# Performance work log

Hardware: AMD Instinct MI355X
Metric: run time of the kernel (lower is better)

Reference implementation:

```python
import jax, jax.numpy as jnp
import numpy as np

BN_EPS = 1e-5

def mish(x):
    return x * jnp.tanh(jax.nn.softplus(x))

def gconv1x1(x, w, b):
    # x: [b, c, h, w]; w: [g, cg, cg] block-diagonal 1x1 grouped conv; b: [c]
    bs, c, h, wd = x.shape
    g, cg, _ = w.shape
    xr = x.reshape(bs, g, cg, h * wd)
    y = jnp.einsum('goi,bgin->bgon', w, xr).reshape(bs, c, h, wd)
    return y + b[None, :, None, None]

def setup_inputs() -> dict:
    key = jax.random.key(0)
    ks = jax.random.split(key, 10)
    bs, c, h, w = 4, 256, 64, 64
    g = 4
    cg = c // g
    s = 0.05
    return {
        'rgb': jax.random.normal(ks[0], (bs, c, h, w), jnp.float32),
        'ir': jax.random.normal(ks[1], (bs, c, h, w), jnp.float32),
        'w_q': jax.random.normal(ks[2], (g, cg, cg), jnp.float32) * s,
        'b_q': jax.random.normal(ks[3], (c,), jnp.float32) * s,
        'w_k': jax.random.normal(ks[4], (g, cg, cg), jnp.float32) * s,
        'b_k': jax.random.normal(ks[5], (c,), jnp.float32) * s,
        'w_v': jax.random.normal(ks[6], (g, cg, cg), jnp.float32) * s,
        'b_v': jax.random.normal(ks[7], (c,), jnp.float32) * s,
        'w4': jax.random.normal(ks[8], (c, c), jnp.float32) * s,
        'b4': jax.random.normal(ks[9], (c,), jnp.float32) * s,
        'gamma': jnp.ones((c,), jnp.float32),
        'beta': jnp.zeros((c,), jnp.float32),
        'rmean': jnp.zeros((c,), jnp.float32),
        'rvar': jnp.ones((c,), jnp.float32),
    }

def reference(rgb, ir, w_q, b_q, w_k, b_k, w_v, b_v, w4, b4, gamma, beta, rmean, rvar):
    bs, c, h, w = rgb.shape
    scale = c ** (-0.5)
    q = gconv1x1(rgb, w_q, b_q).reshape(bs, c, h * w)   # [b, c, n]
    k = gconv1x1(ir, w_k, b_k).reshape(bs, c, h * w)    # [b, c, n]
    v = gconv1x1(ir, w_v, b_v).reshape(bs, c, h * w)    # [b, c, n]
    # attn[b, i, j] = sum_c q[b, c, i] * k[b, c, j]
    attn = jnp.einsum('bci,bcj->bij', q, k) * scale     # [b, n, n]
    attn = jax.nn.softmax(attn, axis=-1)
    z = jnp.einsum('bij,bcj->bci', attn, v)             # [b, c, n]
    z = z.reshape(bs, c, h, w)
    # conv4: full 1x1 conv + BatchNorm (eval stats) + Mish
    y = jnp.einsum('oc,bchw->bohw', w4, z) + b4[None, :, None, None]
    inv = gamma * jax.lax.rsqrt(rvar + BN_EPS)
    y = y * inv[None, :, None, None] + (beta - rmean * inv)[None, :, None, None]
    return rgb + mish(y)
```

## Files before the change

kernel.cpp:

```cpp
#include <hip/hip_runtime.h>
#include <stdint.h>
#include <stddef.h>

typedef short short8 __attribute__((ext_vector_type(8)));
typedef short short4v __attribute__((ext_vector_type(4)));
typedef float f32x4 __attribute__((ext_vector_type(4)));
typedef float f32x16 __attribute__((ext_vector_type(16)));
typedef unsigned int u32x4 __attribute__((ext_vector_type(4)));

#define MFMA16(a, b, c) __builtin_amdgcn_mfma_f32_16x16x32_bf16(a, b, c, 0, 0, 0)
#define MFMA32(a, b, c) __builtin_amdgcn_mfma_f32_32x32x16_bf16(a, b, c, 0, 0, 0)
#define P32SWAP(a, b) asm("v_permlane32_swap_b32 %0, %1" : "+v"(a), "+v"(b))

static constexpr int B = 4, C = 256, CG = 64, N = 4096;

__device__ __forceinline__ unsigned short f2bf(float f) {
  unsigned int u = __builtin_bit_cast(unsigned int, f);
  u += 0x7FFFu + ((u >> 16) & 1u);
  return (unsigned short)(u >> 16);
}

__device__ __forceinline__ void async16(const void* g, void* l) {
  __builtin_amdgcn_global_load_lds(
      (const __attribute__((address_space(1))) unsigned int*)g,
      (__attribute__((address_space(3))) unsigned int*)l, 16, 0, 0);
}

__global__ __launch_bounds__(256) void qkv_kernel(
    const float* __restrict__ rgb, const float* __restrict__ ir,
    const float* __restrict__ wq, const float* __restrict__ bq,
    const float* __restrict__ wk, const float* __restrict__ bk,
    const float* __restrict__ wvv, const float* __restrict__ bvv,
    unsigned short* __restrict__ qT, unsigned short* __restrict__ kT,
    unsigned short* __restrict__ vN) {
  __shared__ unsigned char xTs[256 * 144];
  __shared__ unsigned char wls[64 * 144];

  const int tid = threadIdx.x;
  const int which = blockIdx.z;
  const int bg = blockIdx.y;
  const int b = bg >> 2, g = bg & 3;
  const int n0 = blockIdx.x * 256;

  const float* x = (which == 0) ? rgb : ir;
  const float* w = (which == 0) ? wq : (which == 1 ? wk : wvv);
  const float* bias = (which == 0) ? bq : (which == 1 ? bk : bvv);

  {
    const int p = tid >> 3;
    const int nlo = (tid & 7) * 4;
    const float* r0 = x + ((size_t)(b * C + g * CG + 2 * p) * N + n0 + nlo);
    const float* r1 = r0 + N;
#pragma unroll
    for (int seg = 0; seg < 8; seg++) {
      f32x4 a = *(const f32x4*)(r0 + seg * 32);
      f32x4 c2 = *(const f32x4*)(r1 + seg * 32);
#pragma unroll
      for (int e = 0; e < 4; e++) {
        unsigned int pk =
            (unsigned int)f2bf(a[e]) | ((unsigned int)f2bf(c2[e]) << 16);
        *(unsigned int*)(xTs + (size_t)(seg * 32 + nlo + e) * 144 + 4 * p) = pk;
      }
    }
  }
  {
    const int o = tid >> 2;
    const int cs = (tid & 3) * 16;
    const float* wr = w + (size_t)g * CG * CG + (size_t)o * CG + cs;
#pragma unroll
    for (int i = 0; i < 8; i++) {
      unsigned int pk = (unsigned int)f2bf(wr[2 * i]) |
                        ((unsigned int)f2bf(wr[2 * i + 1]) << 16);
      *(unsigned int*)(wls + (size_t)o * 144 + (cs + 2 * i) * 2) = pk;
    }
  }
  __syncthreads();

  const int wv_ = tid >> 6, lane = tid & 63, l15 = lane & 15, g16 = lane >> 4;
  const f32x4 zero4 = {0.f, 0.f, 0.f, 0.f};
  f32x4 acc[4][4];
#pragma unroll
  for (int i = 0; i < 4; i++)
#pragma unroll
    for (int j = 0; j < 4; j++) acc[i][j] = zero4;

  if (which < 2) {
#pragma unroll
    for (int kk = 0; kk < 2; kk++) {
      short8 af[4], bfr[4];
#pragma unroll
      for (int mt = 0; mt < 4; mt++)
        af[mt] = *(const short8*)(xTs +
                                  (size_t)(wv_ * 64 + mt * 16 + l15) * 144 +
                                  (kk * 32 + 8 * g16) * 2);
#pragma unroll
      for (int nt = 0; nt < 4; nt++)
        bfr[nt] = *(const short8*)(wls + (size_t)(nt * 16 + l15) * 144 +
                                   (kk * 32 + 8 * g16) * 2);
#pragma unroll
      for (int mt = 0; mt < 4; mt++)
#pragma unroll
        for (int nt = 0; nt < 4; nt++)
          acc[mt][nt] = MFMA16(af[mt], bfr[nt], acc[mt][nt]);
    }
    unsigned short* out = (which == 0) ? qT : kT;
    const float qs = (which == 0) ? 0.0625f : 1.0f;
#pragma unroll
    for (int mt = 0; mt < 4; mt++)
#pragma unroll
      for (int nt = 0; nt < 4; nt++)
#pragma unroll
        for (int r = 0; r < 4; r++) {
          int nl = wv_ * 64 + mt * 16 + 4 * g16 + r;
          int co = nt * 16 + l15;
          float val = (acc[mt][nt][r] + bias[g * CG + co]) * qs;
          out[(size_t)(b * N + n0 + nl) * C + g * CG + co] = f2bf(val);
        }
  } else {
#pragma unroll
    for (int kk = 0; kk < 2; kk++) {
      short8 af[4], bfr[4];
#pragma unroll
      for (int mt = 0; mt < 4; mt++)
        af[mt] = *(const short8*)(wls + (size_t)(mt * 16 + l15) * 144 +
                                  (kk * 32 + 8 * g16) * 2);
#pragma unroll
      for (int nt = 0; nt < 4; nt++)
        bfr[nt] = *(const short8*)(xTs +
                                   (size_t)(wv_ * 64 + nt * 16 + l15) * 144 +
                                   (kk * 32 + 8 * g16) * 2);
#pragma unroll
      for (int mt = 0; mt < 4; mt++)
#pragma unroll
        for (int nt = 0; nt < 4; nt++)
          acc[mt][nt] = MFMA16(af[mt], bfr[nt], acc[mt][nt]);
    }
#pragma unroll
    for (int mt = 0; mt < 4; mt++)
#pragma unroll
      for (int nt = 0; nt < 4; nt++)
#pragma unroll
        for (int r = 0; r < 4; r++) {
          int co = mt * 16 + 4 * g16 + r;
          int nl = wv_ * 64 + nt * 16 + l15;
          float val = acc[mt][nt][r] + bias[g * CG + co];
          vN[(size_t)(b * C + g * CG + co) * N + n0 + nl] = f2bf(val);
        }
  }
}

__global__ __launch_bounds__(512, 2) void attn_kernel(
    const unsigned short* __restrict__ qT, const unsigned short* __restrict__ kT,
    const unsigned short* __restrict__ vN, unsigned short* __restrict__ zT) {
  __shared__ __align__(16) unsigned char smem[134144];

  const int tid = threadIdx.x;
  const int pid = blockIdx.x;
  const int lg = (pid & 7) * 32 + (pid >> 3);
  const int b = lg >> 6;
  const int q0 = (lg & 63) * 64;
  const int wv = tid >> 6, lane = tid & 63;
  const int l31 = lane & 31, hj = lane >> 5;
  const int qsub = wv & 1, kvq = wv >> 1;

  unsigned char* Kw = smem + kvq * 32768;
  unsigned char* Vw = Kw + 16384;
  float* zbufA = (float*)smem;
  float* zbufB = (float*)(smem + 66048);
  float* mlb = (float*)(smem + 132096);

  short8 qf[16];
  {
    const unsigned short* qrow =
        qT + (size_t)(b * N + q0 + qsub * 32 + l31) * C + 8 * hj;
#pragma unroll
    for (int kk = 0; kk < 16; kk++) qf[kk] = *(const short8*)(qrow + 16 * kk);
  }

  f32x16 zacc[8];
#pragma unroll
  for (int cs = 0; cs < 8; cs++)
#pragma unroll
    for (int e = 0; e < 16; e++) zacc[cs][e] = 0.f;
  float mr = 4.0f, lsum = 0.f;

  const unsigned short* kq = kT + ((size_t)b * N + kvq * 1024) * C;
  const unsigned short* vq = vN + (size_t)(b * C) * N + kvq * 1024;
  const int t128 = qsub * 64 + lane;
  const int r0 = t128 >> 4;
  const int ccp = t128 & 15;
  const int cl0 = t128 >> 2;
  const int chl = (t128 & 3) ^ ((cl0 >> 1) & 3);

  auto stK = [&](int jt, int h) {
#pragma unroll
    for (int i = 0; i < 4; i++) {
      const unsigned short* src = kq + (size_t)(jt * 32 + i * 8 + r0) * C +
                                  h * 128 + ((ccp ^ r0 ^ ((i & 1) << 3)) << 3);
      async16(src, Kw + h * 8192 + (i * 128 + qsub * 64) * 16);
    }
  };
  auto stV = [&](int jt, int h) {
#pragma unroll
    for (int i = 0; i < 4; i++) {
      const unsigned short* src =
          vq + (size_t)(h * 128 + i * 32 + cl0) * N + jt * 32 + chl * 8;
      async16(src, Vw + h * 8192 + (i * 128 + qsub * 64) * 16);
    }
  };

  const int kxm = l31 & 15;
  const int vxm = (l31 >> 1) & 3;
  unsigned char* krow = Kw + l31 * 256;

  stK(0, 0);
  stK(0, 1);
  stV(0, 0);
  stV(0, 1);
  asm volatile("s_waitcnt vmcnt(0)" ::: "memory");
  __builtin_amdgcn_s_barrier();

  short8 pf0, pf1;
  for (int jt = 0; jt < 32; jt++) {
    asm volatile("s_waitcnt vmcnt(8)" ::: "memory");
    __builtin_amdgcn_s_barrier();
    stV(jt, 1);
    f32x16 s;
#pragma unroll
    for (int e = 0; e < 16; e++) s[e] = 0.f;
#pragma unroll
    for (int kk = 0; kk < 8; kk++) {
      short8 kf =
          *(const short8*)(krow + (((kk * 2 + hj) ^ kxm) << 4));
      s = MFMA32(kf, qf[kk], s);
    }
    asm volatile("s_waitcnt vmcnt(8)" ::: "memory");
    __builtin_amdgcn_s_barrier();
    stK(jt + 1, 0);
#pragma unroll
    for (int kk = 8; kk < 16; kk++) {
      short8 kf = *(const short8*)(krow + 8192 +
                                   ((((kk & 7) * 2 + hj) ^ kxm) << 4));
      s = MFMA32(kf, qf[kk], s);
    }
    asm volatile("s_waitcnt vmcnt(8)" ::: "memory");
    __builtin_amdgcn_s_barrier();
    stK(jt + 1, 1);
    {
      float rmx = s[0];
#pragma unroll
      for (int r = 1; r < 16; r++) rmx = fmaxf(rmx, s[r]);
      rmx = fmaxf(rmx, __shfl_xor(rmx, 32));
      if (__any(rmx > mr + 8.f)) {
        float mn = fmaxf(mr, rmx);
        float al = __expf(mr - mn);
        mr = mn;
        lsum *= al;
#pragma unroll
        for (int cs = 0; cs < 8; cs++) zacc[cs] *= al;
      }
      float psum = 0.f;
#pragma unroll
      for (int r = 0; r < 16; r++) {
        s[r] = __expf(s[r] - mr);
        psum += s[r];
      }
      lsum += psum;
      unsigned int w[8];
#pragma unroll
      for (int e = 0; e < 8; e++)
        w[e] = (unsigned int)f2bf(s[2 * e]) |
               ((unsigned int)f2bf(s[2 * e + 1]) << 16);
      P32SWAP(w[0], w[2]);
      P32SWAP(w[1], w[3]);
      P32SWAP(w[4], w[6]);
      P32SWAP(w[5], w[7]);
      u32x4 t0 = {w[0], w[1], w[2], w[3]};
      u32x4 t1 = {w[4], w[5], w[6], w[7]};
      pf0 = __builtin_bit_cast(short8, t0);
      pf1 = __builtin_bit_cast(short8, t1);
    }
#pragma unroll
    for (int cs = 0; cs < 4; cs++) {
      unsigned char* vr = Vw + (cs * 32 + l31) * 64;
      short8 v0 = *(const short8*)(vr + ((hj ^ vxm) << 4));
      zacc[cs] = MFMA32(v0, pf0, zacc[cs]);
      short8 v1 = *(const short8*)(vr + (((2 + hj) ^ vxm) << 4));
      zacc[cs] = MFMA32(v1, pf1, zacc[cs]);
    }
    asm volatile("s_waitcnt vmcnt(8)" ::: "memory");
    __builtin_amdgcn_s_barrier();
    stV(jt + 1, 0);
#pragma unroll
    for (int cs = 4; cs < 8; cs++) {
      unsigned char* vr = Vw + 8192 + ((cs - 4) * 32 + l31) * 64;
      short8 v0 = *(const short8*)(vr + ((hj ^ vxm) << 4));
      zacc[cs] = MFMA32(v0, pf0, zacc[cs]);
      short8 v1 = *(const short8*)(vr + (((2 + hj) ^ vxm) << 4));
      zacc[cs] = MFMA32(v1, pf1, zacc[cs]);
    }
  }
  asm volatile("s_waitcnt vmcnt(0)" ::: "memory");
  __builtin_amdgcn_s_barrier();

  float ls_tot = lsum + __shfl_xor(lsum, 32);
  if (hj == 0) {
    mlb[(wv * 32 + l31) * 2] = mr;
    mlb[(wv * 32 + l31) * 2 + 1] = ls_tot;
  }
  __syncthreads();
  float mj[4], lj[4];
#pragma unroll
  for (int j = 0; j < 4; j++) {
    int widx = j * 2 + qsub;
    mj[j] = mlb[(widx * 32 + l31) * 2];
    lj[j] = mlb[(widx * 32 + l31) * 2 + 1];
  }
  float M = fmaxf(fmaxf(mj[0], mj[1]), fmaxf(mj[2], mj[3]));
  float L = 0.f;
#pragma unroll
  for (int j = 0; j < 4; j++) L += __expf(mj[j] - M) * lj[j];
  float coef = __expf(mr - M) / L;

  float* buf = (kvq >> 1) ? zbufB : zbufA;
  const int qloc = qsub * 32 + l31;
  if (kvq & 1) {
#pragma unroll
    for (int cs = 0; cs < 8; cs++)
#pragma unroll
      for (int r = 0; r < 16; r++) {
        int c = cs * 32 + (r & 3) + 8 * (r >> 2) + 4 * hj;
        buf[qloc * 258 + c] = coef * zacc[cs][r];
      }
  }
  __syncthreads();
  if (!(kvq & 1)) {
#pragma unroll
    for (int cs = 0; cs < 8; cs++)
#pragma unroll
      for (int r = 0; r < 16; r++) {
        int c = cs * 32 + (r & 3) + 8 * (r >> 2) + 4 * hj;
        float* a = &buf[qloc * 258 + c];
        *a = *a + coef * zacc[cs][r];
      }
  }
  __syncthreads();
  {
    int q = tid >> 3, cseg = (tid & 7) * 32;
    const float* A = zbufA + q * 258 + cseg;
    const float* Bq = zbufB + q * 258 + cseg;
    unsigned short* dst = zT + (size_t)(b * N + q0 + q) * C + cseg;
#pragma unroll
    for (int g = 0; g < 4; g++) {
      unsigned int wo[4];
#pragma unroll
      for (int e = 0; e < 4; e++) {
        float lo = A[g * 8 + 2 * e] + Bq[g * 8 + 2 * e];
        float hi = A[g * 8 + 2 * e + 1] + Bq[g * 8 + 2 * e + 1];
        wo[e] = (unsigned int)f2bf(lo) | ((unsigned int)f2bf(hi) << 16);
      }
      u32x4 tw = {wo[0], wo[1], wo[2], wo[3]};
      *(short8*)(dst + g * 8) = __builtin_bit_cast(short8, tw);
    }
  }
}

__global__ __launch_bounds__(256) void w4prep_kernel(
    const float* __restrict__ w4, unsigned short* __restrict__ w4b) {
  int i = (blockIdx.x * 256 + threadIdx.x) * 4;
  f32x4 v = *(const f32x4*)(w4 + i);
  short4v o;
#pragma unroll
  for (int e = 0; e < 4; e++) o[e] = (short)f2bf(v[e]);
  *(short4v*)(w4b + i) = o;
}

__global__ __launch_bounds__(256) void out_kernel(
    const unsigned short* __restrict__ zT, const unsigned short* __restrict__ w4b,
    const float* __restrict__ b4, const float* __restrict__ gamma,
    const float* __restrict__ beta, const float* __restrict__ rmean,
    const float* __restrict__ rvar, const float* __restrict__ rgb,
    float* __restrict__ out) {
  const int tid = threadIdx.x;
  const int b = blockIdx.y;
  const int n0 = blockIdx.x * 32;
  const int wv_ = tid >> 6, lane = tid & 63, l15 = lane & 15, g16 = lane >> 4;
  const f32x4 zero4 = {0.f, 0.f, 0.f, 0.f};

  f32x4 acc[4][2];
#pragma unroll
  for (int i = 0; i < 4; i++)
#pragma unroll
    for (int j = 0; j < 2; j++) acc[i][j] = zero4;

#pragma unroll
  for (int kk = 0; kk < 8; kk++) {
    short8 bfr[2];
#pragma unroll
    for (int nt = 0; nt < 2; nt++)
      bfr[nt] = *(const short8*)(zT + (size_t)(b * N + n0 + nt * 16 + l15) * C +
                                 kk * 32 + 8 * g16);
    short8 afr[4];
#pragma unroll
    for (int mt = 0; mt < 4; mt++)
      afr[mt] = *(const short8*)(w4b + (size_t)(wv_ * 64 + mt * 16 + l15) * C +
                                 kk * 32 + 8 * g16);
#pragma unroll
    for (int mt = 0; mt < 4; mt++)
#pragma unroll
      for (int nt = 0; nt < 2; nt++)
        acc[mt][nt] = MFMA16(afr[mt], bfr[nt], acc[mt][nt]);
  }

#pragma unroll
  for (int mt = 0; mt < 4; mt++)
#pragma unroll
    for (int r = 0; r < 4; r++) {
      int co = wv_ * 64 + mt * 16 + 4 * g16 + r;
      float bb = b4[co];
      float inv = gamma[co] * rsqrtf(rvar[co] + 1e-5f);
      float sh = beta[co] - rmean[co] * inv;
#pragma unroll
      for (int nt = 0; nt < 2; nt++) {
        int n = n0 + nt * 16 + l15;
        size_t idx = (size_t)(b * C + co) * N + n;
        float yv = acc[mt][nt][r] + bb;
        float tv = yv * inv + sh;
        float s = __expf(fminf(tv, 40.f));
        float u = 1.f + s;
        float u2 = u * u;
        float mish = tv * ((u2 - 1.f) / (u2 + 1.f));
        out[idx] = rgb[idx] + mish;
      }
    }
}

extern "C" void kernel_launch(void* const* d_in, const int* in_sizes, int n_in,
                              void* d_out, int out_size, void* d_ws,
                              size_t ws_size, hipStream_t stream) {
  const float* rgb = (const float*)d_in[0];
  const float* ir = (const float*)d_in[1];
  const float* wq = (const float*)d_in[2];
  const float* bq = (const float*)d_in[3];
  const float* wk = (const float*)d_in[4];
  const float* bk = (const float*)d_in[5];
  const float* wvv = (const float*)d_in[6];
  const float* bvv = (const float*)d_in[7];
  const float* w4 = (const float*)d_in[8];
  const float* b4 = (const float*)d_in[9];
  const float* gamma = (const float*)d_in[10];
  const float* beta = (const float*)d_in[11];
  const float* rmean = (const float*)d_in[12];
  const float* rvar = (const float*)d_in[13];

  unsigned short* qT = (unsigned short*)d_ws;
  unsigned short* kT = qT + (size_t)B * N * C;
  unsigned short* vN = kT + (size_t)B * N * C;
  unsigned short* zT = vN + (size_t)B * N * C;
  unsigned short* w4b = zT + (size_t)B * N * C;

  w4prep_kernel<<<64, 256, 0, stream>>>(w4, w4b);
  qkv_kernel<<<dim3(16, 16, 3), 256, 0, stream>>>(rgb, ir, wq, bq, wk, bk, wvv,
                                                  bvv, qT, kT, vN);
  attn_kernel<<<256, 512, 0, stream>>>(qT, kT, vN, zT);
  out_kernel<<<dim3(128, 4), 256, 0, stream>>>(zT, w4b, b4, gamma, beta, rmean,
                                               rvar, rgb, (float*)d_out);
}
```

Before: 220.1 us.

## Stage epilogue stores through LDS and reorder attention K/V prefetch with priority hints

The projection kernel now writes its q/k and v outputs into shared memory first and then emits coalesced 16-byte global stores, where before each thread wrote scattered 2-byte elements. The output kernel likewise stages results in LDS, precomputes the BN scale and shift per channel, and does vectorized float4 reads of rgb and float4 writes of the output. The attention loop issues the whole next K tile right after the first barrier and the whole next V tile after the second, which drops two barriers per iteration and the barrier before the loop. It also raises wave priority around the MFMA blocks. In exchange it adds extra LDS traffic and __syncthreads in the epilogues, and the attention prefetch schedule now relies on different vmcnt accounting.

Result: no change. 219.0 us (-0.5%).

```diff
diff --git a/kernel.cpp b/kernel.cpp
--- a/kernel.cpp
+++ b/kernel.cpp
@@ -105,6 +105,7 @@
     }
     unsigned short* out = (which == 0) ? qT : kT;
     const float qs = (which == 0) ? 0.0625f : 1.0f;
+    __syncthreads();
 #pragma unroll
     for (int mt = 0; mt < 4; mt++)
 #pragma unroll
@@ -114,8 +115,19 @@
           int nl = wv_ * 64 + mt * 16 + 4 * g16 + r;
           int co = nt * 16 + l15;
           float val = (acc[mt][nt][r] + bias[g * CG + co]) * qs;
-          out[(size_t)(b * N + n0 + nl) * C + g * CG + co] = f2bf(val);
+          *(unsigned short*)(xTs + (size_t)nl * 144 + co * 2) = f2bf(val);
         }
+    __syncthreads();
+    {
+      const int ch = tid & 7;
+      const int rsub = tid >> 3;
+#pragma unroll
+      for (int ro = 0; ro < 8; ro++) {
+        int n = ro * 32 + rsub;
+        short8 d = *(const short8*)(xTs + (size_t)n * 144 + ch * 16);
+        *(short8*)(out + (size_t)(b * N + n0 + n) * C + g * CG + ch * 8) = d;
+      }
+    }
   } else {
 #pragma unroll
     for (int kk = 0; kk < 2; kk++) {
@@ -135,6 +147,7 @@
         for (int nt = 0; nt < 4; nt++)
           acc[mt][nt] = MFMA16(af[mt], bfr[nt], acc[mt][nt]);
     }
+    __syncthreads();
 #pragma unroll
     for (int mt = 0; mt < 4; mt++)
 #pragma unroll
@@ -144,8 +157,19 @@
           int co = mt * 16 + 4 * g16 + r;
           int nl = wv_ * 64 + nt * 16 + l15;
           float val = acc[mt][nt][r] + bias[g * CG + co];
-          vN[(size_t)(b * C + g * CG + co) * N + n0 + nl] = f2bf(val);
+          *(unsigned short*)(xTs + (size_t)co * 528 + nl * 2) = f2bf(val);
         }
+    __syncthreads();
+    {
+      const int ch = tid & 31;
+      const int rsub = tid >> 5;
+#pragma unroll
+      for (int ro = 0; ro < 8; ro++) {
+        int co = ro * 8 + rsub;
+        short8 d = *(const short8*)(xTs + (size_t)co * 528 + ch * 16);
+        *(short8*)(vN + (size_t)(b * C + g * CG + co) * N + n0 + ch * 8) = d;
+      }
+    }
   }
 }
 
@@ -217,35 +241,34 @@
   stK(0, 1);
   stV(0, 0);
   stV(0, 1);
-  asm volatile("s_waitcnt vmcnt(0)" ::: "memory");
-  __builtin_amdgcn_s_barrier();
 
   short8 pf0, pf1;
   for (int jt = 0; jt < 32; jt++) {
     asm volatile("s_waitcnt vmcnt(8)" ::: "memory");
     __builtin_amdgcn_s_barrier();
-    stV(jt, 1);
+    stK(jt + 1, 0);
+    stK(jt + 1, 1);
     f32x16 s;
 #pragma unroll
     for (int e = 0; e < 16; e++) s[e] = 0.f;
+    __builtin_amdgcn_s_setprio(1);
 #pragma unroll
     for (int kk = 0; kk < 8; kk++) {
-      short8 kf =
-          *(const short8*)(krow + (((kk * 2 + hj) ^ kxm) << 4));
+      short8 kf = *(const short8*)(krow + (((kk * 2 + hj) ^ kxm) << 4));
       s = MFMA32(kf, qf[kk], s);
     }
-    asm volatile("s_waitcnt vmcnt(8)" ::: "memory");
-    __builtin_amdgcn_s_barrier();
-    stK(jt + 1, 0);
 #pragma unroll
     for (int kk = 8; kk < 16; kk++) {
       short8 kf = *(const short8*)(krow + 8192 +
                                    ((((kk & 7) * 2 + hj) ^ kxm) << 4));
       s = MFMA32(kf, qf[kk], s);
     }
+    __builtin_amdgcn_s_setprio(0);
+
     asm volatile("s_waitcnt vmcnt(8)" ::: "memory");
     __builtin_amdgcn_s_barrier();
-    stK(jt + 1, 1);
+    stV(jt + 1, 0);
+    stV(jt + 1, 1);
     {
       float rmx = s[0];
 #pragma unroll
@@ -280,6 +303,7 @@
       pf0 = __builtin_bit_cast(short8, t0);
       pf1 = __builtin_bit_cast(short8, t1);
     }
+    __builtin_amdgcn_s_setprio(1);
 #pragma unroll
     for (int cs = 0; cs < 4; cs++) {
       unsigned char* vr = Vw + (cs * 32 + l31) * 64;
@@ -288,9 +312,6 @@
       short8 v1 = *(const short8*)(vr + (((2 + hj) ^ vxm) << 4));
       zacc[cs] = MFMA32(v1, pf1, zacc[cs]);
     }
-    asm volatile("s_waitcnt vmcnt(8)" ::: "memory");
-    __builtin_amdgcn_s_barrier();
-    stV(jt + 1, 0);
 #pragma unroll
     for (int cs = 4; cs < 8; cs++) {
       unsigned char* vr = Vw + 8192 + ((cs - 4) * 32 + l31) * 64;
@@ -299,6 +320,7 @@
       short8 v1 = *(const short8*)(vr + (((2 + hj) ^ vxm) << 4));
       zacc[cs] = MFMA32(v1, pf1, zacc[cs]);
     }
+    __builtin_amdgcn_s_setprio(0);
   }
   asm volatile("s_waitcnt vmcnt(0)" ::: "memory");
   __builtin_amdgcn_s_barrier();
@@ -381,12 +403,22 @@
     const float* __restrict__ beta, const float* __restrict__ rmean,
     const float* __restrict__ rvar, const float* __restrict__ rgb,
     float* __restrict__ out) {
+  __shared__ float yb[256 * 36];
+  __shared__ float invs[256], shbs[256];
+
   const int tid = threadIdx.x;
   const int b = blockIdx.y;
   const int n0 = blockIdx.x * 32;
   const int wv_ = tid >> 6, lane = tid & 63, l15 = lane & 15, g16 = lane >> 4;
   const f32x4 zero4 = {0.f, 0.f, 0.f, 0.f};
 
+  {
+    int co = tid;
+    float inv = gamma[co] * rsqrtf(rvar[co] + 1e-5f);
+    invs[co] = inv;
+    shbs[co] = b4[co] * inv + beta[co] - rmean[co] * inv;
+  }
+
   f32x4 acc[4][2];
 #pragma unroll
   for (int i = 0; i < 4; i++)
@@ -417,22 +449,33 @@
 #pragma unroll
     for (int r = 0; r < 4; r++) {
       int co = wv_ * 64 + mt * 16 + 4 * g16 + r;
-      float bb = b4[co];
-      float inv = gamma[co] * rsqrtf(rvar[co] + 1e-5f);
-      float sh = beta[co] - rmean[co] * inv;
-#pragma unroll
-      for (int nt = 0; nt < 2; nt++) {
-        int n = n0 + nt * 16 + l15;
-        size_t idx = (size_t)(b * C + co) * N + n;
-        float yv = acc[mt][nt][r] + bb;
-        float tv = yv * inv + sh;
+#pragma unroll
+      for (int nt = 0; nt < 2; nt++)
+        yb[co * 36 + nt * 16 + l15] = acc[mt][nt][r];
+    }
+  __syncthreads();
+  {
+    const int ch = tid & 7;
+    const int rsub = tid >> 3;
+#pragma unroll
+    for (int ro = 0; ro < 8; ro++) {
+      int co = ro * 32 + rsub;
+      float inv = invs[co], shb = shbs[co];
+      f32x4 yv = *(const f32x4*)(yb + co * 36 + ch * 4);
+      size_t idx = (size_t)(b * C + co) * N + n0 + ch * 4;
+      f32x4 rg = *(const f32x4*)(rgb + idx);
+      f32x4 o;
+#pragma unroll
+      for (int e = 0; e < 4; e++) {
+        float tv = yv[e] * inv + shb;
         float s = __expf(fminf(tv, 40.f));
         float u = 1.f + s;
         float u2 = u * u;
-        float mish = tv * ((u2 - 1.f) / (u2 + 1.f));
-        out[idx] = rgb[idx] + mish;
-      }
-    }
+        o[e] = rg[e] + tv * ((u2 - 1.f) / (u2 + 1.f));
+      }
+      *(f32x4*)(out + idx) = o;
+    }
+  }
 }
 
 extern "C" void kernel_launch(void* const* d_in, const int* in_sizes, int n_in,
```
